# Performance work log

Hardware: AMD Instinct MI355X
Metric: run time of the kernel (lower is better)

## Reference

```python
import jax, jax.numpy as jnp
import numpy as np

VGG_MEAN = jnp.array([0.485, 0.456, 0.406, 0.5, 0.5, 0.5], dtype=jnp.float32)
VGG_STD = jnp.array([0.229, 0.224, 0.225, 0.1, 0.1, 0.1], dtype=jnp.float32)
KSIZE = 3
STRIDE = 3


def _conv2d(x, w, b, pad):
    y = jax.lax.conv_general_dilated(
        x, w, window_strides=(1, 1), padding=[(pad, pad), (pad, pad)],
        dimension_numbers=("NCHW", "OIHW", "NCHW"))
    return y + b[None, :, None, None]


def _sub_mean(x):
    # MeanShift(1, vgg_mean, vgg_std): (x - mean) / std
    return (x - VGG_MEAN[None, :, None, None]) / VGG_STD[None, :, None, None]


def _feature_extract(x, w1, b1, w2, b2, w3, b3, w4, b4):
    x = jax.nn.relu(_conv2d(x, w1, b1, 1))
    x = jax.nn.relu(_conv2d(x, w2, b2, 1))
    x = jax.nn.relu(_conv2d(x, w3, b3, 1))
    x = _conv2d(x, w4, b4, 0)          # 1x1 conv 128->16 (BasicBlock 'map')
    return jax.nn.leaky_relu(x, 0.2)


def _unfold_k3s3(x):
    # extract_image_patches ksize=3 stride=3 'same'; H,W divisible by 3 -> no pad.
    # Returns [B, C*9, L] with torch.unfold ordering (c, kh, kw) x (row-major L).
    B, C, H, W = x.shape
    Hq, Wq = H // STRIDE, W // STRIDE
    x = x.reshape(B, C, Hq, KSIZE, Wq, KSIZE).transpose(0, 1, 3, 5, 2, 4)
    return x.reshape(B, C * KSIZE * KSIZE, Hq * Wq)


def _l2norm(x, axis):
    n = jnp.sqrt(jnp.sum(x * x, axis=axis, keepdims=True))
    return x / jnp.maximum(n, 1e-12)


def setup_inputs() -> dict:
    key = jax.random.key(0)
    ks = jax.random.split(key, 8)
    B, H, W = 2, 288, 288

    def mkw(k, shape, fan_in):
        return jax.random.normal(k, shape, jnp.float32) * (1.0 / np.sqrt(fan_in))

    return {
        "query": jax.random.normal(ks[0], (B, 6, H, W), jnp.float32),
        "key": jax.random.normal(ks[1], (B, 6, H, W), jnp.float32),
        "flag_8k": 1,
        "w1": mkw(ks[2], (64, 6, 3, 3), 6 * 9),   "b1": jnp.zeros((64,), jnp.float32),
        "w2": mkw(ks[3], (64, 64, 3, 3), 64 * 9), "b2": jnp.zeros((64,), jnp.float32),
        "w3": mkw(ks[4], (128, 64, 3, 3), 64 * 9),"b3": jnp.zeros((128,), jnp.float32),
        "w4": mkw(ks[5], (16, 128, 1, 1), 128),   "b4": jnp.zeros((16,), jnp.float32),
    }


def reference(query, key, flag_8k, w1, b1, w2, b2, w3, b3, w4, b4):
    # flag_8k=1 (static) -> skip bicubic interpolate; scale=1 -> avgpool identity
    q = _sub_mean(query)
    qf = _feature_extract(q, w1, b1, w2, b2, w3, b3, w4, b4)   # [B,16,H,W]
    B, _, H, W = qf.shape

    k = _sub_mean(key)
    kf = _feature_extract(k, w1, b1, w2, b2, w3, b3, w4, b4)   # shared encoder

    qp = _l2norm(_unfold_k3s3(qf), axis=1)                 # [B, 144, M]
    kp = _l2norm(_unfold_k3s3(kf).transpose(0, 2, 1), axis=2)  # [B, L, 144]

    y = jnp.einsum("bld,bdm->blm", kp, qp)                 # [B, L_key, M_query]
    relevance = jnp.max(y, axis=1)                         # [B, M]
    hard_indices = jnp.argmax(y, axis=1)                   # [B, M]
    relevance = relevance.reshape(B, 1, H // STRIDE, W // STRIDE)
    return relevance, hard_indices
```

## Files before the change

### kernel.cpp

```cpp
#include <hip/hip_runtime.h>

#define HH 288
#define WW 288
#define HW (HH*WW)

using f16x8  = __attribute__((ext_vector_type(8))) _Float16;
using f32x4  = __attribute__((ext_vector_type(4))) float;

__device__ __forceinline__ void fma4x8(float acc[4][8], const float4 a, const float4 b0, const float4 b1) {
  float av[4] = {a.x,a.y,a.z,a.w};
  float bv[8] = {b0.x,b0.y,b0.z,b0.w,b1.x,b1.y,b1.z,b1.w};
#pragma unroll
  for (int i=0;i<4;i++)
#pragma unroll
    for (int j=0;j<8;j++)
      acc[i][j] = fmaf(av[i], bv[j], acc[i][j]);
}

__device__ __forceinline__ void fma8x8(float acc[8][8], const float4 a0, const float4 a1,
                                       const float4 b0, const float4 b1) {
  float av[8] = {a0.x,a0.y,a0.z,a0.w,a1.x,a1.y,a1.z,a1.w};
  float bv[8] = {b0.x,b0.y,b0.z,b0.w,b1.x,b1.y,b1.z,b1.w};
#pragma unroll
  for (int i=0;i<8;i++)
#pragma unroll
    for (int j=0;j<8;j++)
      acc[i][j] = fmaf(av[i], bv[j], acc[i][j]);
}

__global__ __launch_bounds__(256) void prep_kernel(const float* __restrict__ w2, const float* __restrict__ w3,
                                                   float* __restrict__ W2t, float* __restrict__ W3t) {
  int tid = blockIdx.x*256 + threadIdx.x;
  int stride = gridDim.x*256;
  for (int e = tid; e < 9*64*64; e += stride) {
    int tap = e / 4096, ci = (e >> 6) & 63, co = e & 63;
    W2t[e] = w2[(co*64 + ci)*9 + tap];
  }
  for (int e = tid; e < 9*64*128; e += stride) {
    int tap = e / 8192, ci = (e >> 7) & 63, co = e & 127;
    W3t[e] = w3[(co*64 + ci)*9 + tap];
  }
}

__global__ __launch_bounds__(256) void conv1_kernel(const float* __restrict__ q, const float* __restrict__ k,
                                                    const float* __restrict__ w1, const float* __restrict__ b1,
                                                    float* __restrict__ X1) {
  __shared__ float Bs[54*128];
  __shared__ float As[54*64];
  __shared__ float bias_s[64];
  int img = blockIdx.z;
  const float* src = (img < 2) ? (q + (size_t)img*6*HW) : (k + (size_t)(img-2)*6*HW);
  int y0 = blockIdx.y*4, x0 = blockIdx.x*32;
  int tid = threadIdx.x;
  for (int e = tid; e < 54*64; e += 256) {
    int kk = e >> 6, co = e & 63;
    int ci = kk/9, tap = kk%9;
    As[e] = w1[(co*6 + ci)*9 + tap];
  }
  if (tid < 64) bias_s[tid] = b1[tid];
  const float mean[6] = {0.485f,0.456f,0.406f,0.5f,0.5f,0.5f};
  const float istd[6] = {1.0f/0.229f,1.0f/0.224f,1.0f/0.225f,10.0f,10.0f,10.0f};
  for (int e = tid; e < 54*128; e += 256) {
    int kk = e >> 7, p = e & 127;
    int ci = kk/9, tap = kk%9;
    int dy = tap/3, dx = tap%3, r = p>>5, xx = p&31;
    int gy = y0 + r + dy - 1, gx = x0 + xx + dx - 1;
    float v = 0.f;
    if (gy >= 0 && gy < HH && gx >= 0 && gx < WW)
      v = (src[(ci*HH + gy)*WW + gx] - mean[ci]) * istd[ci];
    Bs[e] = v;
  }
  __syncthreads();
  int tp = tid & 15, tc = tid >> 4;
  float acc[4][8] = {};
#pragma unroll 6
  for (int kk = 0; kk < 54; kk++) {
    float4 a  = *(float4*)&As[kk*64 + tc*4];
    float4 v0 = *(float4*)&Bs[kk*128 + tp*8];
    float4 v1 = *(float4*)&Bs[kk*128 + tp*8 + 4];
    fma4x8(acc, a, v0, v1);
  }
  int r = tp >> 2, xxb = (tp & 3)*8;
  int gy = y0 + r;
#pragma unroll
  for (int i=0;i<4;i++){
    int co = tc*4 + i;
    float b = bias_s[co];
    float o[8];
#pragma unroll
    for (int j=0;j<8;j++) o[j] = fmaxf(acc[i][j] + b, 0.f);
    float4* dst = (float4*)&X1[((size_t)(img*64+co)*HH + gy)*WW + x0 + xxb];
    dst[0] = make_float4(o[0],o[1],o[2],o[3]);
    dst[1] = make_float4(o[4],o[5],o[6],o[7]);
  }
}

__global__ __launch_bounds__(256) void conv2_kernel(const float* __restrict__ X1, const float* __restrict__ W2t,
                                                    const float* __restrict__ b2, float* __restrict__ X2) {
  __shared__ float Bs[36*128];
  __shared__ float As[36*64];
  __shared__ float bias_s[64];
  int img = blockIdx.z, y0 = blockIdx.y*4, x0 = blockIdx.x*32;
  int tid = threadIdx.x;
  if (tid < 64) bias_s[tid] = b2[tid];
  const float* src = X1 + (size_t)img*64*HW;
  int aoff[9];
#pragma unroll
  for (int j=0;j<9;j++){
    int e = tid + j*256;
    int kk = e >> 6, co = e & 63;
    int ci = kk/9, tap = kk%9;
    aoff[j] = (tap*64 + ci)*64 + co;
  }
  int boff[18];
#pragma unroll
  for (int j=0;j<18;j++){
    int e = tid + j*256;
    int kk = e >> 7, p = e & 127;
    int ci = kk/9, tap = kk%9;
    int dy = tap/3, dx = tap%3, r = p>>5, xx = p&31;
    int gy = y0 + r + dy - 1, gx = x0 + xx + dx - 1;
    bool ok = (gy >= 0 && gy < HH && gx >= 0 && gx < WW);
    boff[j] = ok ? (ci*HW + gy*WW + gx) : -1;
  }
  int tp = tid & 15, tc = tid >> 4;
  float acc[4][8] = {};
  for (int c0 = 0; c0 < 64; c0 += 4) {
    __syncthreads();
#pragma unroll
    for (int j=0;j<9;j++)
      As[tid + j*256] = W2t[aoff[j] + c0*64];
#pragma unroll
    for (int j=0;j<18;j++){
      int o = boff[j];
      Bs[tid + j*256] = (o >= 0) ? src[(size_t)c0*HW + o] : 0.f;
    }
    __syncthreads();
#pragma unroll 6
    for (int kk = 0; kk < 36; kk++) {
      float4 a  = *(float4*)&As[kk*64 + tc*4];
      float4 v0 = *(float4*)&Bs[kk*128 + tp*8];
      float4 v1 = *(float4*)&Bs[kk*128 + tp*8 + 4];
      fma4x8(acc, a, v0, v1);
    }
  }
  int r = tp >> 2, xxb = (tp & 3)*8;
  int gy = y0 + r;
#pragma unroll
  for (int i=0;i<4;i++){
    int co = tc*4 + i;
    float b = bias_s[co];
    float o[8];
#pragma unroll
    for (int j=0;j<8;j++) o[j] = fmaxf(acc[i][j] + b, 0.f);
    float4* dst = (float4*)&X2[((size_t)(img*64+co)*HH + gy)*WW + x0 + xxb];
    dst[0] = make_float4(o[0],o[1],o[2],o[3]);
    dst[1] = make_float4(o[4],o[5],o[6],o[7]);
  }
}

__global__ __launch_bounds__(256) void conv3_kernel(const float* __restrict__ X2, const float* __restrict__ W3t,
                                                    const float* __restrict__ b3, const float* __restrict__ w4,
                                                    const float* __restrict__ b4, float* __restrict__ F) {
  __shared__ float smem[9216];
  __shared__ float w4s[16*128];
  __shared__ float b3s[128];
  __shared__ float b4s[16];
  float* Bs = smem;
  float* As = smem + 4608;
  int img = blockIdx.z, y0 = blockIdx.y*4, x0 = blockIdx.x*32;
  int tid = threadIdx.x;
  for (int e = tid; e < 2048; e += 256) w4s[e] = w4[e];
  if (tid < 128) b3s[tid] = b3[tid];
  if (tid < 16)  b4s[tid] = b4[tid];
  const float* src = X2 + (size_t)img*64*HW;
  int aoff[18];
#pragma unroll
  for (int j=0;j<18;j++){
    int e = tid + j*256;
    int kk = e >> 7, co = e & 127;
    int ci = kk/9, tap = kk%9;
    aoff[j] = (tap*64 + ci)*128 + co;
  }
  int boff[18];
#pragma unroll
  for (int j=0;j<18;j++){
    int e = tid + j*256;
    int kk = e >> 7, p = e & 127;
    int ci = kk/9, tap = kk%9;
    int dy = tap/3, dx = tap%3, r = p>>5, xx = p&31;
    int gy = y0 + r + dy - 1, gx = x0 + xx + dx - 1;
    bool ok = (gy >= 0 && gy < HH && gx >= 0 && gx < WW);
    boff[j] = ok ? (ci*HW + gy*WW + gx) : -1;
  }
  int tp = tid & 15, tc = tid >> 4;
  float acc[8][8] = {};
  for (int c0 = 0; c0 < 64; c0 += 4) {
    __syncthreads();
#pragma unroll
    for (int j=0;j<18;j++)
      As[tid + j*256] = W3t[aoff[j] + c0*128];
#pragma unroll
    for (int j=0;j<18;j++){
      int o = boff[j];
      Bs[tid + j*256] = (o >= 0) ? src[(size_t)c0*HW + o] : 0.f;
    }
    __syncthreads();
#pragma unroll 4
    for (int kk = 0; kk < 36; kk++) {
      float4 a0 = *(float4*)&As[kk*128 + tc*8];
      float4 a1 = *(float4*)&As[kk*128 + tc*8 + 4];
      float4 v0 = *(float4*)&Bs[kk*128 + tp*8];
      float4 v1 = *(float4*)&Bs[kk*128 + tp*8 + 4];
      fma8x8(acc, a0, a1, v0, v1);
    }
  }
#pragma unroll
  for (int i=0;i<8;i++){
    float b = b3s[tc*8+i];
#pragma unroll
    for (int j=0;j<8;j++) acc[i][j] = fmaxf(acc[i][j] + b, 0.f);
  }
  float* red = smem;
  for (int og = 0; og < 4; og++) {
    float pout[4][8];
#pragma unroll
    for (int o=0;o<4;o++){
#pragma unroll
      for (int j=0;j<8;j++){
        float s = 0.f;
#pragma unroll
        for (int i=0;i<8;i++) s = fmaf(w4s[(og*4+o)*128 + tc*8+i], acc[i][j], s);
        pout[o][j] = s;
      }
    }
    __syncthreads();
#pragma unroll
    for (int o=0;o<4;o++)
#pragma unroll
      for (int j=0;j<8;j++)
        red[(o*128 + tp*8+j)*17 + tc] = pout[o][j];
    __syncthreads();
    for (int e = tid; e < 512; e += 256) {
      int o = e >> 7, p = e & 127;
      float s = 0.f;
#pragma unroll
      for (int t=0;t<16;t++) s += red[(o*128+p)*17 + t];
      s += b4s[og*4+o];
      s = (s >= 0.f) ? s : 0.2f*s;
      int pr = p >> 5, px = p & 31;
      F[((size_t)(img*16 + og*4+o)*HH + y0+pr)*WW + x0+px] = s;
    }
  }
}

__global__ __launch_bounds__(256) void unfold_norm_kernel(const float* __restrict__ F, float* __restrict__ P,
                                                          float* __restrict__ Kt,
                                                          _Float16* __restrict__ Ph, _Float16* __restrict__ Pl) {
  __shared__ float tile[16*3*288];
  __shared__ float invn[96];
  int qy = blockIdx.x, img = blockIdx.y, tid = threadIdx.x;
  const float* src = F + (size_t)img*16*HW;
  for (int e = tid; e < 16*3*288; e += 256) {
    int c = e/864, rem = e%864;
    int kh = rem/288, xx = rem%288;
    tile[e] = src[((size_t)c*HH + qy*3+kh)*WW + xx];
  }
  __syncthreads();
  if (tid < 96) {
    float s = 0.f;
    for (int c=0;c<16;c++)
#pragma unroll
      for (int kh=0;kh<3;kh++)
#pragma unroll
        for (int kw=0;kw<3;kw++){
          float v = tile[(c*3+kh)*288 + tid*3+kw];
          s = fmaf(v, v, s);
        }
    invn[tid] = 1.f / fmaxf(sqrtf(s), 1e-12f);
  }
  __syncthreads();
  for (int e = tid; e < 96*160; e += 256) {
    int qx = e/160, d = e%160;
    float v = 0.f;
    if (d < 144) {
      int c = d/9, rem = d%9, kh = rem/3, kw = rem%3;
      v = tile[(c*3+kh)*288 + qx*3+kw] * invn[qx];
    }
    _Float16 hi;
    if (__builtin_fabsf(v) < 6.1035156e-5f) hi = (_Float16)0.f;
    else hi = (_Float16)v;
    float r = v - (float)hi;
    _Float16 lo = (_Float16)(r * 4096.f);
    size_t base = ((size_t)img*9216 + qy*96 + qx)*160 + d;
    Ph[base] = hi;
    Pl[base] = lo;
  }
  if (img < 2) {
    for (int e = tid; e < 96*144; e += 256) {
      int qx = e/144, d = e%144;
      int c = d/9, rem = d%9, kh = rem/3, kw = rem%3;
      P[((size_t)img*9216 + qy*96+qx)*144 + d] = tile[(c*3+kh)*288 + qx*3+kw] * invn[qx];
    }
  } else {
    for (int e = tid; e < 96*144; e += 256) {
      int d = e/96, qx = e%96;
      int c = d/9, rem = d%9, kh = rem/3, kw = rem%3;
      Kt[((size_t)(img-2)*144 + d)*9216 + qy*96 + qx] = tile[(c*3+kh)*288 + qx*3+kw] * invn[qx];
    }
  }
}

__global__ __launch_bounds__(256) void passA_kernel(const _Float16* __restrict__ Ph,
                                                    const _Float16* __restrict__ Pl,
                                                    float* __restrict__ TM) {
  int qg = blockIdx.x, part = blockIdx.y, b = blockIdx.z;
  int tid = threadIdx.x;
  int w = tid >> 6, lane = tid & 63;
  int quad = lane >> 4, lm = lane & 15;
  int m0 = qg*128 + w*32;
  const _Float16* Phq = Ph + (size_t)b*9216*160;
  const _Float16* Plq = Pl + (size_t)b*9216*160;
  const _Float16* Phk = Ph + (size_t)(2+b)*9216*160;
  const _Float16* Plk = Pl + (size_t)(2+b)*9216*160;
  f16x8 qh[2][5], ql[2][5];
#pragma unroll
  for (int ms=0; ms<2; ms++)
#pragma unroll
    for (int kc=0; kc<5; kc++){
      size_t off = (size_t)(m0 + ms*16 + lm)*160 + kc*32 + quad*8;
      qh[ms][kc] = *(const f16x8*)(Phq + off);
      ql[ms][kc] = *(const f16x8*)(Plq + off);
    }
  for (int t = 0; t < 12; t++) {
    int lt = part*12 + t;
    int l0 = lt*128;
    float rmax[2] = {-3e38f, -3e38f};
#pragma unroll
    for (int ls=0; ls<8; ls++){
      size_t rowoff = (size_t)(l0 + ls*16 + lm)*160 + quad*8;
      f32x4 accA[2] = {{0.f,0.f,0.f,0.f},{0.f,0.f,0.f,0.f}};
      f32x4 accB[2] = {{0.f,0.f,0.f,0.f},{0.f,0.f,0.f,0.f}};
#pragma unroll
      for (int kc=0; kc<5; kc++){
        f16x8 ah = *(const f16x8*)(Phk + rowoff + kc*32);
        f16x8 al = *(const f16x8*)(Plk + rowoff + kc*32);
#pragma unroll
        for (int ms=0; ms<2; ms++){
          accA[ms] = __builtin_amdgcn_mfma_f32_16x16x32_f16(ah, qh[ms][kc], accA[ms], 0, 0, 0);
          accB[ms] = __builtin_amdgcn_mfma_f32_16x16x32_f16(ah, ql[ms][kc], accB[ms], 0, 0, 0);
          accB[ms] = __builtin_amdgcn_mfma_f32_16x16x32_f16(al, qh[ms][kc], accB[ms], 0, 0, 0);
        }
      }
#pragma unroll
      for (int ms=0; ms<2; ms++){
        float m01 = fmaxf(accA[ms][0] + accB[ms][0]*2.44140625e-4f,
                          accA[ms][1] + accB[ms][1]*2.44140625e-4f);
        float m23 = fmaxf(accA[ms][2] + accB[ms][2]*2.44140625e-4f,
                          accA[ms][3] + accB[ms][3]*2.44140625e-4f);
        rmax[ms] = fmaxf(rmax[ms], fmaxf(m01, m23));
      }
    }
#pragma unroll
    for (int ms=0; ms<2; ms++){
      float v = rmax[ms];
      v = fmaxf(v, __shfl_xor(v, 16, 64));
      v = fmaxf(v, __shfl_xor(v, 32, 64));
      if (quad == 0) TM[((size_t)(b*72 + lt))*9216 + m0 + ms*16 + lm] = v;
    }
  }
}

__global__ __launch_bounds__(128) void passB_kernel(const float* __restrict__ P,
                                                    const float* __restrict__ Kt,
                                                    const float* __restrict__ TM,
                                                    float* __restrict__ out) {
  __shared__ float qrow[144];
  __shared__ float tmx[72];
  __shared__ float rv[128];
  __shared__ int   ri[128];
  int m = blockIdx.x, b = blockIdx.y, tid = threadIdx.x;
  const float* Q = P + ((size_t)(b*9216) + m)*144;
  const float* Kb = Kt + (size_t)b*144*9216;
  if (tid < 36) *(float4*)&qrow[tid*4] = *(const float4*)&Q[tid*4];
  if (tid < 72) tmx[tid] = TM[((size_t)(b*72 + tid))*9216 + m];
  __syncthreads();
  float M = -3e38f;
#pragma unroll 8
  for (int t = 0; t < 72; t++) M = fmaxf(M, tmx[t]);
  float T = M - 1e-4f;
  float bv = -3e38f; int bi = 0;
  for (int lt = 0; lt < 72; lt++) {
    if (tmx[lt] < T) continue;
    int l = lt*128 + tid;
    float s = 0.f;
#pragma unroll 16
    for (int d = 0; d < 144; d++)
      s = fmaf(Kb[(size_t)d*9216 + l], qrow[d], s);
    if (s > bv) { bv = s; bi = l; }
  }
  rv[tid] = bv; ri[tid] = bi;
  __syncthreads();
  for (int off = 64; off > 0; off >>= 1) {
    if (tid < off) {
      float v2 = rv[tid+off]; int i2 = ri[tid+off];
      if (v2 > rv[tid] || (v2 == rv[tid] && i2 < ri[tid])) { rv[tid] = v2; ri[tid] = i2; }
    }
    __syncthreads();
  }
  if (tid == 0) {
    out[(size_t)b*9216 + m] = rv[0];
    out[2*9216 + (size_t)b*9216 + m] = (float)ri[0];
  }
}

extern "C" void kernel_launch(void* const* d_in, const int* in_sizes, int n_in,
                              void* d_out, int out_size, void* d_ws, size_t ws_size,
                              hipStream_t stream) {
  (void)in_sizes; (void)n_in; (void)out_size; (void)ws_size;
  const float* query = (const float*)d_in[0];
  const float* key   = (const float*)d_in[1];
  const float* w1 = (const float*)d_in[3];
  const float* b1 = (const float*)d_in[4];
  const float* w2 = (const float*)d_in[5];
  const float* b2 = (const float*)d_in[6];
  const float* w3 = (const float*)d_in[7];
  const float* b3 = (const float*)d_in[8];
  const float* w4 = (const float*)d_in[9];
  const float* b4 = (const float*)d_in[10];

  float* ws = (float*)d_ws;
  size_t oX1  = 0;
  size_t oX2  = oX1 + (size_t)4*64*HW;
  size_t oF   = oX2 + (size_t)4*64*HW;
  size_t oP   = oF  + (size_t)4*16*HW;
  size_t oW2t = oP  + (size_t)2*9216*144;
  size_t oW3t = oW2t + (size_t)9*64*64;
  float* X1  = ws + oX1;
  float* X2  = ws + oX2;
  float* F   = ws + oF;
  float* P   = ws + oP;
  float* W2t = ws + oW2t;
  float* W3t = ws + oW3t;
  _Float16* Ph = (_Float16*)(ws + oX1);
  _Float16* Pl = (_Float16*)(ws + oX1 + 3*1024*1024);
  float*    Kt = ws + oX1 + 6*1024*1024;
  float*    TM = ws + oX1 + 9*1024*1024;

  hipLaunchKernelGGL(prep_kernel,        dim3(64),      dim3(256), 0, stream, w2, w3, W2t, W3t);
  hipLaunchKernelGGL(conv1_kernel,       dim3(9,72,4),  dim3(256), 0, stream, query, key, w1, b1, X1);
  hipLaunchKernelGGL(conv2_kernel,       dim3(9,72,4),  dim3(256), 0, stream, X1, W2t, b2, X2);
  hipLaunchKernelGGL(conv3_kernel,       dim3(9,72,4),  dim3(256), 0, stream, X2, W3t, b3, w4, b4, F);
  hipLaunchKernelGGL(unfold_norm_kernel, dim3(96,4),    dim3(256), 0, stream, F, P, Kt, Ph, Pl);
  hipLaunchKernelGGL(passA_kernel,       dim3(72,6,2),  dim3(256), 0, stream, Ph, Pl, TM);
  hipLaunchKernelGGL(passB_kernel,       dim3(9216,2),  dim3(128), 0, stream, P, Kt, TM, (float*)d_out);
}
```

Measured before the change: 1.875 ms.

## Double spatial tile height in conv2/conv3 and simplify im2col staging

Conv2 and conv3 now process 8x32 pixel tiles instead of 4x32. Each thread accumulates 16 pixels per output channel, which halves the grid and raises arithmetic intensity per shared-memory load. The im2col gather replaces 18 precomputed offsets with per-thread row/column masks and a single base offset, which is meant to cut address registers and the bounds logic. The cost is more accumulator registers (128 floats in conv3) and larger shared memory, which can lower occupancy or cause spills.

```diff
diff --git a/kernel.cpp b/kernel.cpp
--- a/kernel.cpp
+++ b/kernel.cpp
@@ -12,17 +12,6 @@
   float bv[8] = {b0.x,b0.y,b0.z,b0.w,b1.x,b1.y,b1.z,b1.w};
 #pragma unroll
   for (int i=0;i<4;i++)
-#pragma unroll
-    for (int j=0;j<8;j++)
-      acc[i][j] = fmaf(av[i], bv[j], acc[i][j]);
-}
-
-__device__ __forceinline__ void fma8x8(float acc[8][8], const float4 a0, const float4 a1,
-                                       const float4 b0, const float4 b1) {
-  float av[8] = {a0.x,a0.y,a0.z,a0.w,a1.x,a1.y,a1.z,a1.w};
-  float bv[8] = {b0.x,b0.y,b0.z,b0.w,b1.x,b1.y,b1.z,b1.w};
-#pragma unroll
-  for (int i=0;i<8;i++)
 #pragma unroll
     for (int j=0;j<8;j++)
       acc[i][j] = fmaf(av[i], bv[j], acc[i][j]);
@@ -97,78 +86,84 @@
 
 __global__ __launch_bounds__(256) void conv2_kernel(const float* __restrict__ X1, const float* __restrict__ W2t,
                                                     const float* __restrict__ b2, float* __restrict__ X2) {
-  __shared__ float Bs[36*128];
+  __shared__ float Bs[36*256];
   __shared__ float As[36*64];
   __shared__ float bias_s[64];
-  int img = blockIdx.z, y0 = blockIdx.y*4, x0 = blockIdx.x*32;
+  int img = blockIdx.z, y0 = blockIdx.y*8, x0 = blockIdx.x*32;
   int tid = threadIdx.x;
   if (tid < 64) bias_s[tid] = b2[tid];
   const float* src = X1 + (size_t)img*64*HW;
   int aoff[9];
 #pragma unroll
   for (int j=0;j<9;j++){
-    int e = tid + j*256;
-    int kk = e >> 6, co = e & 63;
+    int kk = j*4 + (tid>>6);
     int ci = kk/9, tap = kk%9;
-    aoff[j] = (tap*64 + ci)*64 + co;
-  }
-  int boff[18];
-#pragma unroll
-  for (int j=0;j<18;j++){
-    int e = tid + j*256;
-    int kk = e >> 7, p = e & 127;
-    int ci = kk/9, tap = kk%9;
-    int dy = tap/3, dx = tap%3, r = p>>5, xx = p&31;
-    int gy = y0 + r + dy - 1, gx = x0 + xx + dx - 1;
-    bool ok = (gy >= 0 && gy < HH && gx >= 0 && gx < WW);
-    boff[j] = ok ? (ci*HW + gy*WW + gx) : -1;
-  }
+    aoff[j] = (tap*64 + ci)*64 + (tid&63);
+  }
+  int pr = tid>>5, pc = tid&31;
+  int gy0 = y0 + pr - 1, gx0 = x0 + pc - 1;
+  bool rm[3], cm[3];
+#pragma unroll
+  for (int d=0; d<3; d++){ rm[d] = (unsigned)(gy0+d) < HH; cm[d] = (unsigned)(gx0+d) < WW; }
+  long base = (long)gy0*WW + gx0;
   int tp = tid & 15, tc = tid >> 4;
-  float acc[4][8] = {};
+  float acc[4][16] = {};
   for (int c0 = 0; c0 < 64; c0 += 4) {
     __syncthreads();
 #pragma unroll
     for (int j=0;j<9;j++)
       As[tid + j*256] = W2t[aoff[j] + c0*64];
 #pragma unroll
-    for (int j=0;j<18;j++){
-      int o = boff[j];
-      Bs[tid + j*256] = (o >= 0) ? src[(size_t)c0*HW + o] : 0.f;
-    }
-    __syncthreads();
-#pragma unroll 6
+    for (int j=0;j<36;j++){
+      const int ci = j/9, tap = j%9, dy = tap/3, dx = tap%3;
+      float v = 0.f;
+      if (rm[dy] && cm[dx])
+        v = src[(long)(c0+ci)*HW + base + dy*WW + dx];
+      Bs[j*256 + tid] = v;
+    }
+    __syncthreads();
+#pragma unroll 4
     for (int kk = 0; kk < 36; kk++) {
       float4 a  = *(float4*)&As[kk*64 + tc*4];
-      float4 v0 = *(float4*)&Bs[kk*128 + tp*8];
-      float4 v1 = *(float4*)&Bs[kk*128 + tp*8 + 4];
-      fma4x8(acc, a, v0, v1);
-    }
-  }
-  int r = tp >> 2, xxb = (tp & 3)*8;
-  int gy = y0 + r;
+      float4 v0 = *(float4*)&Bs[kk*256 + tp*16];
+      float4 v1 = *(float4*)&Bs[kk*256 + tp*16 + 4];
+      float4 v2 = *(float4*)&Bs[kk*256 + tp*16 + 8];
+      float4 v3 = *(float4*)&Bs[kk*256 + tp*16 + 12];
+      float av[4] = {a.x,a.y,a.z,a.w};
+      float bv[16] = {v0.x,v0.y,v0.z,v0.w, v1.x,v1.y,v1.z,v1.w,
+                      v2.x,v2.y,v2.z,v2.w, v3.x,v3.y,v3.z,v3.w};
+#pragma unroll
+      for (int i=0;i<4;i++)
+#pragma unroll
+        for (int jj=0;jj<16;jj++)
+          acc[i][jj] = fmaf(av[i], bv[jj], acc[i][jj]);
+    }
+  }
+  int gy = y0 + (tp>>1), xb = x0 + (tp&1)*16;
 #pragma unroll
   for (int i=0;i<4;i++){
     int co = tc*4 + i;
     float b = bias_s[co];
-    float o[8];
-#pragma unroll
-    for (int j=0;j<8;j++) o[j] = fmaxf(acc[i][j] + b, 0.f);
-    float4* dst = (float4*)&X2[((size_t)(img*64+co)*HH + gy)*WW + x0 + xxb];
+    float o[16];
+#pragma unroll
+    for (int jj=0;jj<16;jj++) o[jj] = fmaxf(acc[i][jj] + b, 0.f);
+    float4* dst = (float4*)&X2[((size_t)(img*64+co)*HH + gy)*WW + xb];
     dst[0] = make_float4(o[0],o[1],o[2],o[3]);
     dst[1] = make_float4(o[4],o[5],o[6],o[7]);
+    dst[2] = make_float4(o[8],o[9],o[10],o[11]);
+    dst[3] = make_float4(o[12],o[13],o[14],o[15]);
   }
 }
 
 __global__ __launch_bounds__(256) void conv3_kernel(const float* __restrict__ X2, const float* __restrict__ W3t,
                                                     const float* __restrict__ b3, const float* __restrict__ w4,
                                                     const float* __restrict__ b4, float* __restrict__ F) {
-  __shared__ float smem[9216];
-  __shared__ float w4s[16*128];
+  __shared__ float Bs[36*256];
+  __shared__ float As[36*128];
+  __shared__ float w4s[2048];
   __shared__ float b3s[128];
   __shared__ float b4s[16];
-  float* Bs = smem;
-  float* As = smem + 4608;
-  int img = blockIdx.z, y0 = blockIdx.y*4, x0 = blockIdx.x*32;
+  int img = blockIdx.z, y0 = blockIdx.y*8, x0 = blockIdx.x*32;
   int tid = threadIdx.x;
   for (int e = tid; e < 2048; e += 256) w4s[e] = w4[e];
   if (tid < 128) b3s[tid] = b3[tid];
@@ -177,79 +172,84 @@
   int aoff[18];
 #pragma unroll
   for (int j=0;j<18;j++){
-    int e = tid + j*256;
-    int kk = e >> 7, co = e & 127;
+    int kk = j*2 + (tid>>7);
     int ci = kk/9, tap = kk%9;
-    aoff[j] = (tap*64 + ci)*128 + co;
-  }
-  int boff[18];
-#pragma unroll
-  for (int j=0;j<18;j++){
-    int e = tid + j*256;
-    int kk = e >> 7, p = e & 127;
-    int ci = kk/9, tap = kk%9;
-    int dy = tap/3, dx = tap%3, r = p>>5, xx = p&31;
-    int gy = y0 + r + dy - 1, gx = x0 + xx + dx - 1;
-    bool ok = (gy >= 0 && gy < HH && gx >= 0 && gx < WW);
-    boff[j] = ok ? (ci*HW + gy*WW + gx) : -1;
-  }
+    aoff[j] = (tap*64 + ci)*128 + (tid&127);
+  }
+  int pr = tid>>5, pc = tid&31;
+  int gy0 = y0 + pr - 1, gx0 = x0 + pc - 1;
+  bool rm[3], cm[3];
+#pragma unroll
+  for (int d=0; d<3; d++){ rm[d] = (unsigned)(gy0+d) < HH; cm[d] = (unsigned)(gx0+d) < WW; }
+  long base = (long)gy0*WW + gx0;
   int tp = tid & 15, tc = tid >> 4;
-  float acc[8][8] = {};
+  float acc[8][16] = {};
   for (int c0 = 0; c0 < 64; c0 += 4) {
     __syncthreads();
 #pragma unroll
     for (int j=0;j<18;j++)
       As[tid + j*256] = W3t[aoff[j] + c0*128];
 #pragma unroll
-    for (int j=0;j<18;j++){
-      int o = boff[j];
-      Bs[tid + j*256] = (o >= 0) ? src[(size_t)c0*HW + o] : 0.f;
-    }
-    __syncthreads();
-#pragma unroll 4
+    for (int j=0;j<36;j++){
+      const int ci = j/9, tap = j%9, dy = tap/3, dx = tap%3;
+      float v = 0.f;
+      if (rm[dy] && cm[dx])
+        v = src[(long)(c0+ci)*HW + base + dy*WW + dx];
+      Bs[j*256 + tid] = v;
+    }
+    __syncthreads();
+#pragma unroll 2
     for (int kk = 0; kk < 36; kk++) {
       float4 a0 = *(float4*)&As[kk*128 + tc*8];
       float4 a1 = *(float4*)&As[kk*128 + tc*8 + 4];
-      float4 v0 = *(float4*)&Bs[kk*128 + tp*8];
-      float4 v1 = *(float4*)&Bs[kk*128 + tp*8 + 4];
-      fma8x8(acc, a0, a1, v0, v1);
+      float4 v0 = *(float4*)&Bs[kk*256 + tp*16];
+      float4 v1 = *(float4*)&Bs[kk*256 + tp*16 + 4];
+      float4 v2 = *(float4*)&Bs[kk*256 + tp*16 + 8];
+      float4 v3 = *(float4*)&Bs[kk*256 + tp*16 + 12];
+      float av[8] = {a0.x,a0.y,a0.z,a0.w, a1.x,a1.y,a1.z,a1.w};
+      float bv[16] = {v0.x,v0.y,v0.z,v0.w, v1.x,v1.y,v1.z,v1.w,
+                      v2.x,v2.y,v2.z,v2.w, v3.x,v3.y,v3.z,v3.w};
+#pragma unroll
+      for (int i=0;i<8;i++)
+#pragma unroll
+        for (int jj=0;jj<16;jj++)
+          acc[i][jj] = fmaf(av[i], bv[jj], acc[i][jj]);
     }
   }
 #pragma unroll
   for (int i=0;i<8;i++){
     float b = b3s[tc*8+i];
 #pragma unroll
-    for (int j=0;j<8;j++) acc[i][j] = fmaxf(acc[i][j] + b, 0.f);
-  }
-  float* red = smem;
-  for (int og = 0; og < 4; og++) {
-    float pout[4][8];
-#pragma unroll
-    for (int o=0;o<4;o++){
-#pragma unroll
-      for (int j=0;j<8;j++){
+    for (int jj=0;jj<16;jj++) acc[i][jj] = fmaxf(acc[i][jj] + b, 0.f);
+  }
+  float* red = Bs;
+  for (int op = 0; op < 8; op++) {
+    float pout[2][16];
+#pragma unroll
+    for (int oo=0;oo<2;oo++)
+#pragma unroll
+      for (int jj=0;jj<16;jj++){
         float s = 0.f;
 #pragma unroll
-        for (int i=0;i<8;i++) s = fmaf(w4s[(og*4+o)*128 + tc*8+i], acc[i][j], s);
-        pout[o][j] = s;
+        for (int i=0;i<8;i++) s = fmaf(w4s[(op*2+oo)*128 + tc*8+i], acc[i][jj], s);
+        pout[oo][jj] = s;
       }
-    }
-    __syncthreads();
-#pragma unroll
-    for (int o=0;o<4;o++)
-#pragma unroll
-      for (int j=0;j<8;j++)
-        red[(o*128 + tp*8+j)*17 + tc] = pout[o][j];
+    __syncthreads();
+#pragma unroll
+    for (int oo=0;oo<2;oo++)
+#pragma unroll
+      for (int jj=0;jj<16;jj++)
+        red[(oo*256 + tp*16+jj)*17 + tc] = pout[oo][jj];
     __syncthreads();
     for (int e = tid; e < 512; e += 256) {
-      int o = e >> 7, p = e & 127;
+      int oo = e >> 8, p = e & 255;
       float s = 0.f;
 #pragma unroll
-      for (int t=0;t<16;t++) s += red[(o*128+p)*17 + t];
-      s += b4s[og*4+o];
+      for (int t=0;t<16;t++) s += red[(oo*256+p)*17 + t];
+      int o = op*2 + oo;
+      s += b4s[o];
       s = (s >= 0.f) ? s : 0.2f*s;
-      int pr = p >> 5, px = p & 31;
-      F[((size_t)(img*16 + og*4+o)*HH + y0+pr)*WW + x0+px] = s;
+      F[((size_t)(img*16 + o)*HH + y0 + (p>>5))*WW + x0 + (p&31)] = s;
     }
   }
 }
@@ -343,13 +343,13 @@
       f32x4 accB[2] = {{0.f,0.f,0.f,0.f},{0.f,0.f,0.f,0.f}};
 #pragma unroll
       for (int kc=0; kc<5; kc++){
-        f16x8 ah = *(const f16x8*)(Phk + rowoff + kc*32);
-        f16x8 al = *(const f16x8*)(Plk + rowoff + kc*32);
+        f16x8 ahv = *(const f16x8*)(Phk + rowoff + kc*32);
+        f16x8 alv = *(const f16x8*)(Plk + rowoff + kc*32);
 #pragma unroll
         for (int ms=0; ms<2; ms++){
-          accA[ms] = __builtin_amdgcn_mfma_f32_16x16x32_f16(ah, qh[ms][kc], accA[ms], 0, 0, 0);
-          accB[ms] = __builtin_amdgcn_mfma_f32_16x16x32_f16(ah, ql[ms][kc], accB[ms], 0, 0, 0);
-          accB[ms] = __builtin_amdgcn_mfma_f32_16x16x32_f16(al, qh[ms][kc], accB[ms], 0, 0, 0);
+          accA[ms] = __builtin_amdgcn_mfma_f32_16x16x32_f16(ahv, qh[ms][kc], accA[ms], 0, 0, 0);
+          accB[ms] = __builtin_amdgcn_mfma_f32_16x16x32_f16(ahv, ql[ms][kc], accB[ms], 0, 0, 0);
+          accB[ms] = __builtin_amdgcn_mfma_f32_16x16x32_f16(alv, qh[ms][kc], accB[ms], 0, 0, 0);
         }
       }
 #pragma unroll
@@ -449,8 +449,8 @@
 
   hipLaunchKernelGGL(prep_kernel,        dim3(64),      dim3(256), 0, stream, w2, w3, W2t, W3t);
   hipLaunchKernelGGL(conv1_kernel,       dim3(9,72,4),  dim3(256), 0, stream, query, key, w1, b1, X1);
-  hipLaunchKernelGGL(conv2_kernel,       dim3(9,72,4),  dim3(256), 0, stream, X1, W2t, b2, X2);
-  hipLaunchKernelGGL(conv3_kernel,       dim3(9,72,4),  dim3(256), 0, stream, X2, W3t, b3, w4, b4, F);
+  hipLaunchKernelGGL(conv2_kernel,       dim3(9,36,4),  dim3(256), 0, stream, X1, W2t, b2, X2);
+  hipLaunchKernelGGL(conv3_kernel,       dim3(9,36,4),  dim3(256), 0, stream, X2, W3t, b3, w4, b4, F);
   hipLaunchKernelGGL(unfold_norm_kernel, dim3(96,4),    dim3(256), 0, stream, F, P, Kt, Ph, Pl);
   hipLaunchKernelGGL(passA_kernel,       dim3(72,6,2),  dim3(256), 0, stream, Ph, Pl, TM);
   hipLaunchKernelGGL(passB_kernel,       dim3(9216,2),  dim3(128), 0, stream, P, Kt, TM, (float*)d_out);
```

New measurement: 2.269 ms. 21.1% more time.
